# Kernel tuning notes

Measured on AMD Instinct MI355X. Metric: run time of the kernel, lower is better.

The kernel has to match this reference:

```python
import jax, jax.numpy as jnp
import numpy as np

# --- constants matching the torch module's default-camera / material / light setup ---
IMAGE_SIZE = 128
SCALE = 1.0
FOCAL = 12.0
R_MAT = jnp.array([[-1.0, 0.0, 0.0], [0.0, 1.0, 0.0], [0.0, 0.0, -1.0]], dtype=jnp.float32)
T_VEC = jnp.array([0.0, 0.0, 2.0 * SCALE], dtype=jnp.float32)
CAM_POS = jnp.array([0.0, 0.0, 2.0 * SCALE], dtype=jnp.float32)  # camera center in world coords
LIGHT_LOC = jnp.array([0.0, 1.0, 3.0], dtype=jnp.float32)
AMB_L, DIFF_L, SPEC_L = 0.5, 0.3, 0.2          # PointLights defaults
MAT_AMB, MAT_DIFF, MAT_SPEC = 1.0, 1.0, 0.6    # Materials(specular_color=0.6)
SHININESS = 10.0
TEXEL = jnp.array([142.0, 179.0, 247.0], dtype=jnp.float32) / 255.0  # uniform vertex color
BG = 1.0  # BlendParams background
EPS = 1e-8


def _normalize(v):
    return v / (jnp.linalg.norm(v, axis=-1, keepdims=True) + EPS)


def _render_one(verts, faces):
    """verts: [V,3] world space; faces: [F,3] int. Returns ([3,H,W] rgb*255, [1,H,W] alpha)."""
    H = W = IMAGE_SIZE
    # world -> view (PyTorch3D row-vector convention: x_view = x @ R + T)
    view = verts @ R_MAT + T_VEC              # [V,3]
    z = view[:, 2]                            # [V] view-space depth (>0 in front)
    ndc = FOCAL * view[:, :2] / z[:, None]    # [V,2] perspective projection to NDC
    tri = ndc[faces]                          # [F,3,2]
    tz = z[faces]                             # [F,3]

    # pixel centers in NDC (PyTorch3D: +x left, +y up)
    xs = 1.0 - (2.0 * jnp.arange(W) + 1.0) / W
    ys = 1.0 - (2.0 * jnp.arange(H) + 1.0) / H
    gy, gx = jnp.meshgrid(ys, xs, indexing='ij')
    px = gx.reshape(-1).astype(jnp.float32)   # [P]
    py = gy.reshape(-1).astype(jnp.float32)   # [P]

    v0, v1, v2 = tri[:, 0], tri[:, 1], tri[:, 2]   # [F,2]

    def edge(a, b):  # signed area cross(b-a, p-a) for all pixels -> [P,F]
        return ((b[:, 0] - a[:, 0])[None] * (py[:, None] - a[:, 1][None])
                - (b[:, 1] - a[:, 1])[None] * (px[:, None] - a[:, 0][None]))

    area = ((v1[:, 0] - v0[:, 0]) * (v2[:, 1] - v0[:, 1])
            - (v1[:, 1] - v0[:, 1]) * (v2[:, 0] - v0[:, 0]))   # [F]
    area_safe = jnp.where(jnp.abs(area) < EPS, EPS, area)
    b0 = edge(v1, v2) / area_safe             # [P,F]
    b1 = edge(v2, v0) / area_safe
    b2 = 1.0 - b0 - b1
    inside = (b0 >= 0) & (b1 >= 0) & (b2 >= 0) & (jnp.abs(area) > EPS)[None]

    # perspective-correct interpolated depth: z_pix = 1 / sum_i(b_i / z_i)
    S = b0 / tz[:, 0] + b1 / tz[:, 1] + b2 / tz[:, 2]
    depth = jnp.where(inside & (S > EPS), 1.0 / jnp.maximum(S, EPS), jnp.inf)
    fidx = jnp.argmin(depth, axis=1)          # [P] z-buffer winner (faces_per_pixel=1)
    hit = jnp.isfinite(jnp.min(depth, axis=1))

    # --- recompute barycentrics only for the winning face per pixel (cheap, [P]) ---
    f = faces[fidx]                           # [P,3]
    tv = ndc[f]                               # [P,3,2]
    tzp = z[f]                                # [P,3]
    a0, a1, a2 = tv[:, 0], tv[:, 1], tv[:, 2]

    def edge_p(a, b):
        return (b[:, 0] - a[:, 0]) * (py - a[:, 1]) - (b[:, 1] - a[:, 1]) * (px - a[:, 0])

    ar = (a1[:, 0] - a0[:, 0]) * (a2[:, 1] - a0[:, 1]) - (a1[:, 1] - a0[:, 1]) * (a2[:, 0] - a0[:, 0])
    ar = jnp.where(jnp.abs(ar) < EPS, EPS, ar)
    bb0 = edge_p(a1, a2) / ar
    bb1 = edge_p(a2, a0) / ar
    bb2 = 1.0 - bb0 - bb1
    w = jnp.stack([bb0 / tzp[:, 0], bb1 / tzp[:, 1], bb2 / tzp[:, 2]], axis=-1)
    pc = w / (jnp.sum(w, axis=-1, keepdims=True) + EPS)   # [P,3] perspective-correct barycentrics

    # --- vertex normals (world space) ---
    fv = verts[faces]                         # [F,3,3]
    fn = jnp.cross(fv[:, 1] - fv[:, 0], fv[:, 2] - fv[:, 0])  # [F,3]
    vn = (jnp.zeros_like(verts)
          .at[faces[:, 0]].add(fn)
          .at[faces[:, 1]].add(fn)
          .at[faces[:, 2]].add(fn))
    vn = _normalize(vn)

    # --- interpolate position/normal, Phong shade ---
    pos = jnp.einsum('pk,pkd->pd', pc, verts[f])   # [P,3]
    nrm = _normalize(jnp.einsum('pk,pkd->pd', pc, vn[f]))
    l = _normalize(LIGHT_LOC - pos)
    vdir = _normalize(CAM_POS - pos)
    ndl = jax.nn.relu(jnp.sum(nrm * l, axis=-1))          # [P]
    refl = 2.0 * jnp.sum(nrm * l, axis=-1, keepdims=True) * nrm - l
    spec_cos = jax.nn.relu(jnp.sum(refl * vdir, axis=-1))
    ambient = AMB_L * MAT_AMB
    diffuse = DIFF_L * MAT_DIFF * ndl
    specular = SPEC_L * MAT_SPEC * spec_cos ** SHININESS
    color = TEXEL[None] * (ambient + diffuse[:, None]) + specular[:, None]

    rgb = jnp.where(hit[:, None], color, BG)              # hard blend with white bg
    alpha = hit.astype(verts.dtype)
    img = rgb.reshape(H, W, 3).transpose(2, 0, 1) * 255.0  # [3,H,W]
    a = alpha.reshape(1, H, W)
    return img, a


def setup_inputs() -> dict:
    key = jax.random.key(0)
    k1, k2 = jax.random.split(key)
    B, V, F = 2, 1300, 2500
    vertices = jax.random.normal(k1, (B, V, 3), dtype=jnp.float32) * 0.05  # head-scale mesh near origin
    faces = jax.random.randint(k2, (F, 3), 0, V, dtype=jnp.int32)
    return {"vertices": vertices, "faces": faces}


def reference(vertices, faces):
    # ori_size == image_size, so the area-interpolation in the torch module is the identity.
    images, alphas = jax.lax.map(lambda v: _render_one(v, faces), vertices)
    return images, alphas
```

## Files before the change

### kernel.cpp

```cpp
#include <hip/hip_runtime.h>
#include <math.h>

#pragma clang fp contract(off)

#define IMG_H 128
#define IMG_W 128
#define HW (IMG_H * IMG_W)
#define NB 2
#define NV 1300
#define NF 2500
#define EPSF 1e-8f
#define NCHUNK 32
#define CHUNK ((NF + NCHUNK - 1) / NCHUNK)
#define NBLK 4096

#define OFF_FACE 31232
#define OFF_DBUF 351488

#define DINIT 0x7F800000FFFFFFFFull

__device__ __forceinline__ float bcastf(float v, int s) {
    return __int_as_float(__builtin_amdgcn_readlane(__float_as_int(v), s));
}

__global__ __launch_bounds__(256) void k_face(const float* __restrict__ verts,
                                              const int* __restrict__ faces,
                                              float* __restrict__ vn,
                                              float4* __restrict__ face) {
    int i = blockIdx.x * 256 + threadIdx.x;
    if (i >= NB * NF) return;
    int b = i / NF;
    int f = i - b * NF;
    int i0 = faces[f * 3 + 0];
    int i1 = faces[f * 3 + 1];
    int i2 = faces[f * 3 + 2];
    const float* wv = verts + (size_t)b * NV * 3;
    float v0x = wv[i0 * 3 + 0], v0y = wv[i0 * 3 + 1], v0z = wv[i0 * 3 + 2];
    float v1x = wv[i1 * 3 + 0], v1y = wv[i1 * 3 + 1], v1z = wv[i1 * 3 + 2];
    float v2x = wv[i2 * 3 + 0], v2y = wv[i2 * 3 + 1], v2z = wv[i2 * 3 + 2];
    float z0 = 2.0f - v0z, z1 = 2.0f - v1z, z2 = 2.0f - v2z;
    float p0x = (12.0f * (-v0x)) / z0, p0y = (12.0f * v0y) / z0;
    float p1x = (12.0f * (-v1x)) / z1, p1y = (12.0f * v1y) / z1;
    float p2x = (12.0f * (-v2x)) / z2, p2y = (12.0f * v2y) / z2;

    float t1 = (p1x - p0x) * (p2y - p0y);
    float t2 = (p1y - p0y) * (p2x - p0x);
    float area = t1 - t2;
    float aabs = fabsf(area);
    float area_safe = (aabs < EPSF) ? EPSF : area;
    bool valid = aabs > EPSF;
    float minx, maxx, miny, maxy;
    if (valid) {
        minx = fminf(p0x, fminf(p1x, p2x)) - 1e-3f;
        maxx = fmaxf(p0x, fmaxf(p1x, p2x)) + 1e-3f;
        miny = fminf(p0y, fminf(p1y, p2y)) - 1e-3f;
        maxy = fmaxf(p0y, fmaxf(p1y, p2y)) + 1e-3f;
    } else {
        minx = 1e30f; maxx = -1e30f; miny = 1e30f; maxy = -1e30f;
    }
    int o = b * NF + f;
    face[0 * NB * NF + o] = make_float4(p2x - p1x, p2y - p1y, p1x, p1y);
    face[1 * NB * NF + o] = make_float4(p0x - p2x, p0y - p2y, p2x, p2y);
    face[2 * NB * NF + o] = make_float4(area_safe, z0, z1, z2);
    face[3 * NB * NF + o] = make_float4(minx, maxx, miny, maxy);

    float ax = v1x - v0x, ay = v1y - v0y, az = v1z - v0z;
    float bx = v2x - v0x, by = v2y - v0y, bz = v2z - v0z;
    float fnx = ay * bz - az * by;
    float fny = az * bx - ax * bz;
    float fnz = ax * by - ay * bx;
    float* vnb = vn + (size_t)b * NV * 3;
    atomicAdd(&vnb[i0 * 3 + 0], fnx);
    atomicAdd(&vnb[i0 * 3 + 1], fny);
    atomicAdd(&vnb[i0 * 3 + 2], fnz);
    atomicAdd(&vnb[i1 * 3 + 0], fnx);
    atomicAdd(&vnb[i1 * 3 + 1], fny);
    atomicAdd(&vnb[i1 * 3 + 2], fnz);
    atomicAdd(&vnb[i2 * 3 + 0], fnx);
    atomicAdd(&vnb[i2 * 3 + 1], fny);
    atomicAdd(&vnb[i2 * 3 + 2], fnz);
}

__global__ __launch_bounds__(256) void k_raster(const float4* __restrict__ face,
                                                unsigned long long* __restrict__ dbuf) {
    int t = threadIdx.x;
    int wid = t >> 6, lid = t & 63;
    int bx = blockIdx.x;

    int chunk = ((bx & 7) << 2) | wid;
    int b = (bx >> 3) & 1;
    int tile = (bx >> 4) & 1;
    int reg = bx >> 5;
    int r0 = (reg >> 3) * 8;
    int c0 = (reg & 7) * 16;
    int cw0 = c0 + tile * 8;
    int f0 = chunk * CHUNK;
    int nf = NF - f0; if (nf > CHUNK) nf = CHUNK;

    float txhi = 1.0f - (2.0f * (float)cw0 + 1.0f) / 128.0f;
    float txlo = 1.0f - (2.0f * (float)(cw0 + 7) + 1.0f) / 128.0f;
    float tyhi = 1.0f - (2.0f * (float)r0 + 1.0f) / 128.0f;
    float tylo = 1.0f - (2.0f * (float)(r0 + 7) + 1.0f) / 128.0f;

    const float4* pE0 = face + (size_t)(0 * NB + b) * NF + f0;
    const float4* pE1 = face + (size_t)(1 * NB + b) * NF + f0;
    const float4* pFD = face + (size_t)(2 * NB + b) * NF + f0;
    const float4* pBB = face + (size_t)(3 * NB + b) * NF + f0;

    int r = r0 + (lid >> 3);
    int c = cw0 + (lid & 7);
    int p = r * IMG_W + c;
    float px = 1.0f - (2.0f * (float)c + 1.0f) / 128.0f;
    float py = 1.0f - (2.0f * (float)r + 1.0f) / 128.0f;

    unsigned long long best = DINIT;

    for (int base = 0; base < nf; base += 64) {
        int tt = base + lid;
        int fi = (tt < nf) ? tt : (nf - 1);
        float4 bb = pBB[fi];
        float4 E0 = pE0[fi];
        float4 E1 = pE1[fi];
        float4 FD = pFD[fi];
        bool pass = false;
        if (tt < nf) {
            pass = (bb.y >= txlo) && (bb.x <= txhi) && (bb.w >= tylo) && (bb.z <= tyhi);
            if (pass) {
                float as = FD.x;
                float u0l = E0.x * (tylo - E0.w), u0h = E0.x * (tyhi - E0.w);
                float u0mn = fminf(u0l, u0h), u0mx = fmaxf(u0l, u0h);
                float u1l = E1.x * (tylo - E1.w), u1h = E1.x * (tyhi - E1.w);
                float u1mn = fminf(u1l, u1h), u1mx = fmaxf(u1l, u1h);
                float v0l = E0.y * (txlo - E0.z), v0h = E0.y * (txhi - E0.z);
                float v0mn = fminf(v0l, v0h), v0mx = fmaxf(v0l, v0h);
                float v1l = E1.y * (txlo - E1.z), v1h = E1.y * (txhi - E1.z);
                float v1mn = fminf(v1l, v1h), v1mx = fmaxf(v1l, v1h);
                float e0mx = u0mx - v0mn, e0mn = u0mn - v0mx;
                float e1mx = u1mx - v1mn, e1mn = u1mn - v1mx;
                const float DL = 1e-4f;
                if (as > 0.0f) {
                    pass = (e0mx >= -DL) && (e1mx >= -DL) && (((as - e0mn) - e1mn) >= -DL);
                } else {
                    pass = (e0mn <= DL) && (e1mn <= DL) && (((as - e0mx) - e1mx) <= DL);
                }
            }
        }
        unsigned long long m = __ballot(pass);
        while (m) {
            int s = (int)__builtin_ctzll(m);
            m &= m - 1;
            float bmnx = bcastf(bb.x, s), bmxx = bcastf(bb.y, s);
            float bmny = bcastf(bb.z, s), bmxy = bcastf(bb.w, s);
            if (px >= bmnx && px <= bmxx && py >= bmny && py <= bmxy) {
                float e0x = bcastf(E0.x, s), e0y = bcastf(E0.y, s);
                float e0z = bcastf(E0.z, s), e0w = bcastf(E0.w, s);
                float e1x = bcastf(E1.x, s), e1y = bcastf(E1.y, s);
                float e1z = bcastf(E1.z, s), e1w = bcastf(E1.w, s);
                float as  = bcastf(FD.x, s), fz0 = bcastf(FD.y, s);
                float fz1 = bcastf(FD.z, s), fz2 = bcastf(FD.w, s);
                float u1 = e0x * (py - e0w);
                float u2 = e0y * (px - e0z);
                float e0 = u1 - u2;
                float u3 = e1x * (py - e1w);
                float u4 = e1y * (px - e1z);
                float e1 = u3 - u4;
                bool ok = (as > 0.0f) ? (e0 >= 0.0f && e1 >= 0.0f)
                                      : (e0 <= 0.0f && e1 <= 0.0f);
                if (ok) {
                    float b0 = e0 / as;
                    float b1 = e1 / as;
                    float b2 = (1.0f - b0) - b1;
                    if (b2 >= 0.0f) {
                        float S = ((b0 / fz0) + (b1 / fz1)) + (b2 / fz2);
                        if (S > EPSF) {
                            float depth = 1.0f / fmaxf(S, EPSF);
                            unsigned long long pk =
                                ((unsigned long long)__float_as_uint(depth) << 32) |
                                (unsigned)(f0 + base + s);
                            if (pk < best) best = pk;
                        }
                    }
                }
            }
        }
    }
    dbuf[((size_t)chunk * NB + b) * HW + p] = best;
}

__global__ __launch_bounds__(256) void k_shade(const float* __restrict__ verts,
                                               const int* __restrict__ faces,
                                               const float* __restrict__ vn,
                                               const unsigned long long* __restrict__ dbuf,
                                               float* __restrict__ out) {
    int i = blockIdx.x * 256 + threadIdx.x;
    int b = i >> 14;
    int p = i & (HW - 1);
    unsigned long long pk = DINIT;
    for (int k = 0; k < NCHUNK; ++k) {
        unsigned long long v = dbuf[((size_t)k * NB + b) * HW + p];
        if (v < pk) pk = v;
    }
    unsigned dbits = (unsigned)(pk >> 32);
    bool hit = dbits < 0x7F800000u;
    float cr = 255.0f, cg = 255.0f, cb = 255.0f, alpha = 0.0f;
    if (hit) {
        alpha = 1.0f;
        int f = (int)(unsigned)(pk & 0xFFFFFFFFull);
        int row = p >> 7;
        int col = p & 127;
        float px = 1.0f - (2.0f * (float)col + 1.0f) / 128.0f;
        float py = 1.0f - (2.0f * (float)row + 1.0f) / 128.0f;
        int i0 = faces[f * 3 + 0];
        int i1 = faces[f * 3 + 1];
        int i2 = faces[f * 3 + 2];
        const float* wv = verts + (size_t)b * NV * 3;
        float v0x = wv[i0 * 3 + 0], v0y = wv[i0 * 3 + 1], v0z = wv[i0 * 3 + 2];
        float v1x = wv[i1 * 3 + 0], v1y = wv[i1 * 3 + 1], v1z = wv[i1 * 3 + 2];
        float v2x = wv[i2 * 3 + 0], v2y = wv[i2 * 3 + 1], v2z = wv[i2 * 3 + 2];
        float z0 = 2.0f - v0z, z1 = 2.0f - v1z, z2 = 2.0f - v2z;
        float a0x = (12.0f * (-v0x)) / z0, a0y = (12.0f * v0y) / z0;
        float a1x = (12.0f * (-v1x)) / z1, a1y = (12.0f * v1y) / z1;
        float a2x = (12.0f * (-v2x)) / z2, a2y = (12.0f * v2y) / z2;

        float t1 = (a1x - a0x) * (a2y - a0y);
        float t2 = (a1y - a0y) * (a2x - a0x);
        float ar = t1 - t2;
        ar = (fabsf(ar) < EPSF) ? EPSF : ar;
        float u1 = (a2x - a1x) * (py - a1y);
        float u2 = (a2y - a1y) * (px - a1x);
        float bb0 = (u1 - u2) / ar;
        float u3 = (a0x - a2x) * (py - a2y);
        float u4 = (a0y - a2y) * (px - a2x);
        float bb1 = (u3 - u4) / ar;
        float bb2 = (1.0f - bb0) - bb1;
        float w0 = bb0 / z0;
        float w1 = bb1 / z1;
        float w2 = bb2 / z2;
        float denom = ((w0 + w1) + w2) + EPSF;
        float pc0 = w0 / denom;
        float pc1 = w1 / denom;
        float pc2 = w2 / denom;

        float posx = (pc0 * v0x + pc1 * v1x) + pc2 * v2x;
        float posy = (pc0 * v0y + pc1 * v1y) + pc2 * v2y;
        float posz = (pc0 * v0z + pc1 * v1z) + pc2 * v2z;

        const float* vnb = vn + (size_t)b * NV * 3;
        float n0x = vnb[i0 * 3 + 0], n0y = vnb[i0 * 3 + 1], n0z = vnb[i0 * 3 + 2];
        float n1x = vnb[i1 * 3 + 0], n1y = vnb[i1 * 3 + 1], n1z = vnb[i1 * 3 + 2];
        float n2x = vnb[i2 * 3 + 0], n2y = vnb[i2 * 3 + 1], n2z = vnb[i2 * 3 + 2];
        float in0 = 1.0f / (sqrtf(n0x * n0x + n0y * n0y + n0z * n0z) + EPSF);
        float in1 = 1.0f / (sqrtf(n1x * n1x + n1y * n1y + n1z * n1z) + EPSF);
        float in2 = 1.0f / (sqrtf(n2x * n2x + n2y * n2y + n2z * n2z) + EPSF);
        n0x *= in0; n0y *= in0; n0z *= in0;
        n1x *= in1; n1y *= in1; n1z *= in1;
        n2x *= in2; n2y *= in2; n2z *= in2;
        float nx = (pc0 * n0x + pc1 * n1x) + pc2 * n2x;
        float ny = (pc0 * n0y + pc1 * n1y) + pc2 * n2y;
        float nz = (pc0 * n0z + pc1 * n1z) + pc2 * n2z;
        float inn = 1.0f / (sqrtf(nx * nx + ny * ny + nz * nz) + EPSF);
        nx *= inn; ny *= inn; nz *= inn;

        float lx = 0.0f - posx, ly = 1.0f - posy, lz = 3.0f - posz;
        float iln = 1.0f / (sqrtf(lx * lx + ly * ly + lz * lz) + EPSF);
        lx *= iln; ly *= iln; lz *= iln;
        float vx = 0.0f - posx, vy = 0.0f - posy, vz = 2.0f - posz;
        float ivn = 1.0f / (sqrtf(vx * vx + vy * vy + vz * vz) + EPSF);
        vx *= ivn; vy *= ivn; vz *= ivn;

        float ndl = nx * lx + ny * ly + nz * lz;
        float ndlr = fmaxf(ndl, 0.0f);
        float rx = 2.0f * ndl * nx - lx;
        float ry = 2.0f * ndl * ny - ly;
        float rz = 2.0f * ndl * nz - lz;
        float sc = fmaxf(rx * vx + ry * vy + rz * vz, 0.0f);
        float spec = 0.2f * 0.6f * powf(sc, 10.0f);
        float shade = 0.5f * 1.0f + 0.3f * 1.0f * ndlr;
        cr = ((142.0f / 255.0f) * shade + spec) * 255.0f;
        cg = ((179.0f / 255.0f) * shade + spec) * 255.0f;
        cb = ((247.0f / 255.0f) * shade + spec) * 255.0f;
    }
    float* img = out + (size_t)b * 3 * HW;
    img[0 * HW + p] = cr;
    img[1 * HW + p] = cg;
    img[2 * HW + p] = cb;
    out[(size_t)NB * 3 * HW + (size_t)b * HW + p] = alpha;
}

extern "C" void kernel_launch(void* const* d_in, const int* in_sizes, int n_in,
                              void* d_out, int out_size, void* d_ws, size_t ws_size,
                              hipStream_t stream) {
    const float* verts = (const float*)d_in[0];
    const int* faces = (const int*)d_in[1];
    char* ws = (char*)d_ws;
    float* vn = (float*)(ws + 0);
    float4* face = (float4*)(ws + OFF_FACE);
    unsigned long long* dbuf = (unsigned long long*)(ws + OFF_DBUF);
    float* out = (float*)d_out;

    hipMemsetAsync(vn, 0, NB * NV * 3 * sizeof(float), stream);
    k_face<<<(NB * NF + 255) / 256, 256, 0, stream>>>(verts, faces, vn, face);
    k_raster<<<NBLK, 256, 0, stream>>>(face, dbuf);
    k_shade<<<(NB * HW) / 256, 256, 0, stream>>>(verts, faces, vn, dbuf, out);
}
```

Before: 109.4 us.

## Bin faces into screen regions and rasterize only each region's face list

k_face now computes which 16x16 pixel regions each valid face's bounding box overlaps. It appends the face index to a per-region bin through atomic counters. k_raster no longer scans fixed face chunks: each block walks one region's bin, split into 8 slices, and loads edge and depth data only for faces that pass the tile bbox test. The per-chunk depth buffer shrinks from 32 slices to 8, so k_shade reads less. The cost is atomic contention during binning, extra workspace, and load imbalance between blocks when face counts differ per region.

```diff
diff --git a/kernel.cpp b/kernel.cpp
--- a/kernel.cpp
+++ b/kernel.cpp
@@ -10,12 +10,14 @@
 #define NV 1300
 #define NF 2500
 #define EPSF 1e-8f
-#define NCHUNK 32
-#define CHUNK ((NF + NCHUNK - 1) / NCHUNK)
-#define NBLK 4096
-
-#define OFF_FACE 31232
-#define OFF_DBUF 351488
+#define NREG 64
+#define KSL 8
+#define NBLK (NREG * NB * KSL)
+
+#define OFF_CNT 31200
+#define OFF_FACE 31712
+#define OFF_BIN 351712
+#define OFF_DBUF 991712
 
 #define DINIT 0x7F800000FFFFFFFFull
 
@@ -26,7 +28,9 @@
 __global__ __launch_bounds__(256) void k_face(const float* __restrict__ verts,
                                               const int* __restrict__ faces,
                                               float* __restrict__ vn,
-                                              float4* __restrict__ face) {
+                                              float4* __restrict__ face,
+                                              int* __restrict__ cnt,
+                                              unsigned short* __restrict__ bin) {
     int i = blockIdx.x * 256 + threadIdx.x;
     if (i >= NB * NF) return;
     int b = i / NF;
@@ -79,53 +83,82 @@
     atomicAdd(&vnb[i2 * 3 + 0], fnx);
     atomicAdd(&vnb[i2 * 3 + 1], fny);
     atomicAdd(&vnb[i2 * 3 + 2], fnz);
+
+    if (!valid) return;
+    float rxmin_f = (128.0f * (1.0f - maxx) - 31.0f) / 32.0f;
+    float rxmax_f = (128.0f * (1.0f - minx) - 1.0f) / 32.0f;
+    float rymin_f = (128.0f * (1.0f - maxy) - 31.0f) / 32.0f;
+    float rymax_f = (128.0f * (1.0f - miny) - 1.0f) / 32.0f;
+    rxmin_f = fminf(fmaxf(rxmin_f, -1.0f), 8.0f);
+    rxmax_f = fminf(fmaxf(rxmax_f, -1.0f), 8.0f);
+    rymin_f = fminf(fmaxf(rymin_f, -1.0f), 8.0f);
+    rymax_f = fminf(fmaxf(rymax_f, -1.0f), 8.0f);
+    int rx0 = (int)ceilf(rxmin_f - 1e-4f); if (rx0 < 0) rx0 = 0;
+    int rx1 = (int)floorf(rxmax_f + 1e-4f); if (rx1 > 7) rx1 = 7;
+    int ry0 = (int)ceilf(rymin_f - 1e-4f); if (ry0 < 0) ry0 = 0;
+    int ry1 = (int)floorf(rymax_f + 1e-4f); if (ry1 > 7) ry1 = 7;
+    for (int ry = ry0; ry <= ry1; ++ry) {
+        for (int rx = rx0; rx <= rx1; ++rx) {
+            int reg = ry * 8 + rx;
+            int pos = atomicAdd(&cnt[b * NREG + reg], 1);
+            bin[((size_t)b * NREG + reg) * NF + pos] = (unsigned short)f;
+        }
+    }
 }
 
 __global__ __launch_bounds__(256) void k_raster(const float4* __restrict__ face,
+                                                const int* __restrict__ cnt,
+                                                const unsigned short* __restrict__ bin,
                                                 unsigned long long* __restrict__ dbuf) {
     int t = threadIdx.x;
     int wid = t >> 6, lid = t & 63;
     int bx = blockIdx.x;
 
-    int chunk = ((bx & 7) << 2) | wid;
+    int k = bx & (KSL - 1);
     int b = (bx >> 3) & 1;
-    int tile = (bx >> 4) & 1;
-    int reg = bx >> 5;
-    int r0 = (reg >> 3) * 8;
+    int reg = bx >> 4;
+    int r0 = (reg >> 3) * 16;
     int c0 = (reg & 7) * 16;
-    int cw0 = c0 + tile * 8;
-    int f0 = chunk * CHUNK;
-    int nf = NF - f0; if (nf > CHUNK) nf = CHUNK;
-
-    float txhi = 1.0f - (2.0f * (float)cw0 + 1.0f) / 128.0f;
-    float txlo = 1.0f - (2.0f * (float)(cw0 + 7) + 1.0f) / 128.0f;
-    float tyhi = 1.0f - (2.0f * (float)r0 + 1.0f) / 128.0f;
-    float tylo = 1.0f - (2.0f * (float)(r0 + 7) + 1.0f) / 128.0f;
-
-    const float4* pE0 = face + (size_t)(0 * NB + b) * NF + f0;
-    const float4* pE1 = face + (size_t)(1 * NB + b) * NF + f0;
-    const float4* pFD = face + (size_t)(2 * NB + b) * NF + f0;
-    const float4* pBB = face + (size_t)(3 * NB + b) * NF + f0;
-
-    int r = r0 + (lid >> 3);
-    int c = cw0 + (lid & 7);
+    int r0w = r0 + (wid >> 1) * 8;
+    int c0w = c0 + (wid & 1) * 8;
+
+    int n = cnt[b * NREG + reg];
+    int len = (n + KSL - 1) / KSL;
+    int start = k * len; if (start > n) start = n;
+    int end = start + len; if (end > n) end = n;
+
+    float txhi = 1.0f - (2.0f * (float)c0w + 1.0f) / 128.0f;
+    float txlo = 1.0f - (2.0f * (float)(c0w + 7) + 1.0f) / 128.0f;
+    float tyhi = 1.0f - (2.0f * (float)r0w + 1.0f) / 128.0f;
+    float tylo = 1.0f - (2.0f * (float)(r0w + 7) + 1.0f) / 128.0f;
+
+    const float4* pE0 = face + (size_t)(0 * NB + b) * NF;
+    const float4* pE1 = face + (size_t)(1 * NB + b) * NF;
+    const float4* pFD = face + (size_t)(2 * NB + b) * NF;
+    const float4* pBB = face + (size_t)(3 * NB + b) * NF;
+    const unsigned short* pbin = bin + ((size_t)b * NREG + reg) * NF;
+
+    int r = r0w + (lid >> 3);
+    int c = c0w + (lid & 7);
     int p = r * IMG_W + c;
     float px = 1.0f - (2.0f * (float)c + 1.0f) / 128.0f;
     float py = 1.0f - (2.0f * (float)r + 1.0f) / 128.0f;
 
     unsigned long long best = DINIT;
 
-    for (int base = 0; base < nf; base += 64) {
-        int tt = base + lid;
-        int fi = (tt < nf) ? tt : (nf - 1);
+    for (int base = start; base < end; base += 64) {
+        int ii = base + lid;
+        int jj = (ii < end) ? ii : (end - 1);
+        int fi = (int)pbin[jj];
         float4 bb = pBB[fi];
-        float4 E0 = pE0[fi];
-        float4 E1 = pE1[fi];
-        float4 FD = pFD[fi];
         bool pass = false;
-        if (tt < nf) {
+        float4 E0, E1, FD;
+        if (ii < end) {
             pass = (bb.y >= txlo) && (bb.x <= txhi) && (bb.w >= tylo) && (bb.z <= tyhi);
             if (pass) {
+                E0 = pE0[fi];
+                E1 = pE1[fi];
+                FD = pFD[fi];
                 float as = FD.x;
                 float u0l = E0.x * (tylo - E0.w), u0h = E0.x * (tyhi - E0.w);
                 float u0mn = fminf(u0l, u0h), u0mx = fmaxf(u0l, u0h);
@@ -158,6 +191,7 @@
                 float e1z = bcastf(E1.z, s), e1w = bcastf(E1.w, s);
                 float as  = bcastf(FD.x, s), fz0 = bcastf(FD.y, s);
                 float fz1 = bcastf(FD.z, s), fz2 = bcastf(FD.w, s);
+                int fcand = __builtin_amdgcn_readlane(fi, s);
                 float u1 = e0x * (py - e0w);
                 float u2 = e0y * (px - e0z);
                 float e0 = u1 - u2;
@@ -176,7 +210,7 @@
                             float depth = 1.0f / fmaxf(S, EPSF);
                             unsigned long long pk =
                                 ((unsigned long long)__float_as_uint(depth) << 32) |
-                                (unsigned)(f0 + base + s);
+                                (unsigned)fcand;
                             if (pk < best) best = pk;
                         }
                     }
@@ -184,7 +218,7 @@
             }
         }
     }
-    dbuf[((size_t)chunk * NB + b) * HW + p] = best;
+    dbuf[((size_t)k * NB + b) * HW + p] = best;
 }
 
 __global__ __launch_bounds__(256) void k_shade(const float* __restrict__ verts,
@@ -196,7 +230,7 @@
     int b = i >> 14;
     int p = i & (HW - 1);
     unsigned long long pk = DINIT;
-    for (int k = 0; k < NCHUNK; ++k) {
+    for (int k = 0; k < KSL; ++k) {
         unsigned long long v = dbuf[((size_t)k * NB + b) * HW + p];
         if (v < pk) pk = v;
     }
@@ -294,12 +328,14 @@
     const int* faces = (const int*)d_in[1];
     char* ws = (char*)d_ws;
     float* vn = (float*)(ws + 0);
+    int* cnt = (int*)(ws + OFF_CNT);
     float4* face = (float4*)(ws + OFF_FACE);
+    unsigned short* bin = (unsigned short*)(ws + OFF_BIN);
     unsigned long long* dbuf = (unsigned long long*)(ws + OFF_DBUF);
     float* out = (float*)d_out;
 
-    hipMemsetAsync(vn, 0, NB * NV * 3 * sizeof(float), stream);
-    k_face<<<(NB * NF + 255) / 256, 256, 0, stream>>>(verts, faces, vn, face);
-    k_raster<<<NBLK, 256, 0, stream>>>(face, dbuf);
+    hipMemsetAsync(ws, 0, OFF_CNT + NB * NREG * sizeof(int), stream);
+    k_face<<<(NB * NF + 255) / 256, 256, 0, stream>>>(verts, faces, vn, face, cnt, bin);
+    k_raster<<<NBLK, 256, 0, stream>>>(face, cnt, bin, dbuf);
     k_shade<<<(NB * HW) / 256, 256, 0, stream>>>(verts, faces, vn, dbuf, out);
 }
```

Result: slower. 221.0 us (+102.1%).

## Rasterize 16x8 tiles per wave with two pixels per lane

Applied to the files above, without the earlier changes.

Each wave now covers a 16x8 pixel region instead of 8x8, so every lane handles two pixels (rows r and r+4) that share the column-dependent edge terms. The block count is halved, so face data loading, the coarse tile culling and the ballot loop run half as many times per pixel. The cost is a coarser per-tile cull, which lets more faces through to the per-pixel tests, and higher register pressure from the duplicated per-pixel work.

```diff
diff --git a/kernel.cpp b/kernel.cpp
--- a/kernel.cpp
+++ b/kernel.cpp
@@ -12,7 +12,8 @@
 #define EPSF 1e-8f
 #define NCHUNK 32
 #define CHUNK ((NF + NCHUNK - 1) / NCHUNK)
-#define NBLK 4096
+#define NREG 128
+#define NBLK 2048
 
 #define OFF_FACE 31232
 #define OFF_DBUF 351488
@@ -89,16 +90,14 @@
 
     int chunk = ((bx & 7) << 2) | wid;
     int b = (bx >> 3) & 1;
-    int tile = (bx >> 4) & 1;
-    int reg = bx >> 5;
+    int reg = bx >> 4;
     int r0 = (reg >> 3) * 8;
     int c0 = (reg & 7) * 16;
-    int cw0 = c0 + tile * 8;
     int f0 = chunk * CHUNK;
     int nf = NF - f0; if (nf > CHUNK) nf = CHUNK;
 
-    float txhi = 1.0f - (2.0f * (float)cw0 + 1.0f) / 128.0f;
-    float txlo = 1.0f - (2.0f * (float)(cw0 + 7) + 1.0f) / 128.0f;
+    float txhi = 1.0f - (2.0f * (float)c0 + 1.0f) / 128.0f;
+    float txlo = 1.0f - (2.0f * (float)(c0 + 15) + 1.0f) / 128.0f;
     float tyhi = 1.0f - (2.0f * (float)r0 + 1.0f) / 128.0f;
     float tylo = 1.0f - (2.0f * (float)(r0 + 7) + 1.0f) / 128.0f;
 
@@ -107,13 +106,17 @@
     const float4* pFD = face + (size_t)(2 * NB + b) * NF + f0;
     const float4* pBB = face + (size_t)(3 * NB + b) * NF + f0;
 
-    int r = r0 + (lid >> 3);
-    int c = cw0 + (lid & 7);
-    int p = r * IMG_W + c;
+    int c = c0 + (lid & 15);
+    int ra = r0 + (lid >> 4);
+    int rb = ra + 4;
+    int pa = ra * IMG_W + c;
+    int pb = rb * IMG_W + c;
     float px = 1.0f - (2.0f * (float)c + 1.0f) / 128.0f;
-    float py = 1.0f - (2.0f * (float)r + 1.0f) / 128.0f;
-
-    unsigned long long best = DINIT;
+    float pya = 1.0f - (2.0f * (float)ra + 1.0f) / 128.0f;
+    float pyb = 1.0f - (2.0f * (float)rb + 1.0f) / 128.0f;
+
+    unsigned long long besta = DINIT;
+    unsigned long long bestb = DINIT;
 
     for (int base = 0; base < nf; base += 64) {
         int tt = base + lid;
@@ -151,40 +154,69 @@
             m &= m - 1;
             float bmnx = bcastf(bb.x, s), bmxx = bcastf(bb.y, s);
             float bmny = bcastf(bb.z, s), bmxy = bcastf(bb.w, s);
-            if (px >= bmnx && px <= bmxx && py >= bmny && py <= bmxy) {
+            bool inx = (px >= bmnx) && (px <= bmxx);
+            bool ina = inx && (pya >= bmny) && (pya <= bmxy);
+            bool inb = inx && (pyb >= bmny) && (pyb <= bmxy);
+            if (ina || inb) {
                 float e0x = bcastf(E0.x, s), e0y = bcastf(E0.y, s);
                 float e0z = bcastf(E0.z, s), e0w = bcastf(E0.w, s);
                 float e1x = bcastf(E1.x, s), e1y = bcastf(E1.y, s);
                 float e1z = bcastf(E1.z, s), e1w = bcastf(E1.w, s);
                 float as  = bcastf(FD.x, s), fz0 = bcastf(FD.y, s);
                 float fz1 = bcastf(FD.z, s), fz2 = bcastf(FD.w, s);
-                float u1 = e0x * (py - e0w);
+                unsigned fidx = (unsigned)(f0 + base + s);
                 float u2 = e0y * (px - e0z);
-                float e0 = u1 - u2;
-                float u3 = e1x * (py - e1w);
                 float u4 = e1y * (px - e1z);
-                float e1 = u3 - u4;
-                bool ok = (as > 0.0f) ? (e0 >= 0.0f && e1 >= 0.0f)
-                                      : (e0 <= 0.0f && e1 <= 0.0f);
-                if (ok) {
-                    float b0 = e0 / as;
-                    float b1 = e1 / as;
-                    float b2 = (1.0f - b0) - b1;
-                    if (b2 >= 0.0f) {
-                        float S = ((b0 / fz0) + (b1 / fz1)) + (b2 / fz2);
-                        if (S > EPSF) {
-                            float depth = 1.0f / fmaxf(S, EPSF);
-                            unsigned long long pk =
-                                ((unsigned long long)__float_as_uint(depth) << 32) |
-                                (unsigned)(f0 + base + s);
-                            if (pk < best) best = pk;
+                if (ina) {
+                    float u1 = e0x * (pya - e0w);
+                    float e0 = u1 - u2;
+                    float u3 = e1x * (pya - e1w);
+                    float e1 = u3 - u4;
+                    bool ok = (as > 0.0f) ? (e0 >= 0.0f && e1 >= 0.0f)
+                                          : (e0 <= 0.0f && e1 <= 0.0f);
+                    if (ok) {
+                        float b0 = e0 / as;
+                        float b1 = e1 / as;
+                        float b2 = (1.0f - b0) - b1;
+                        if (b2 >= 0.0f) {
+                            float S = ((b0 / fz0) + (b1 / fz1)) + (b2 / fz2);
+                            if (S > EPSF) {
+                                float depth = 1.0f / fmaxf(S, EPSF);
+                                unsigned long long pk =
+                                    ((unsigned long long)__float_as_uint(depth) << 32) | fidx;
+                                if (pk < besta) besta = pk;
+                            }
+                        }
+                    }
+                }
+                if (inb) {
+                    float u1 = e0x * (pyb - e0w);
+                    float e0 = u1 - u2;
+                    float u3 = e1x * (pyb - e1w);
+                    float e1 = u3 - u4;
+                    bool ok = (as > 0.0f) ? (e0 >= 0.0f && e1 >= 0.0f)
+                                          : (e0 <= 0.0f && e1 <= 0.0f);
+                    if (ok) {
+                        float b0 = e0 / as;
+                        float b1 = e1 / as;
+                        float b2 = (1.0f - b0) - b1;
+                        if (b2 >= 0.0f) {
+                            float S = ((b0 / fz0) + (b1 / fz1)) + (b2 / fz2);
+                            if (S > EPSF) {
+                                float depth = 1.0f / fmaxf(S, EPSF);
+                                unsigned long long pk =
+                                    ((unsigned long long)__float_as_uint(depth) << 32) | fidx;
+                                if (pk < bestb) bestb = pk;
+                            }
                         }
                     }
                 }
             }
         }
     }
-    dbuf[((size_t)chunk * NB + b) * HW + p] = best;
+    unsigned long long* dslab = dbuf + ((size_t)chunk * NB + b) * HW;
+    dslab[pa] = besta;
+    dslab[pb] = bestb;
 }
 
 __global__ __launch_bounds__(256) void k_shade(const float* __restrict__ verts,
```

After: 117.2 us. 1.07x slower.
